# Optimization experiments

Hardware: AMD Instinct MI355X
Metric: run time of the kernel (lower is better)

## Reference

```python
import jax, jax.numpy as jnp
import numpy as np

B, N, D, H = 2, 2048, 1024, 16
HD = D // H

def setup_inputs() -> dict:
    key = jax.random.key(0)
    ks = jax.random.split(key, 8)
    s = lambda fan_in: 1.0 / np.sqrt(fan_in)
    return {
        "x": jax.random.normal(ks[0], (B, N, D), jnp.float32),
        "coverage": jax.random.uniform(ks[1], (B, N, 1), jnp.float32),
        "w_qkv": jax.random.normal(ks[2], (D, 3 * D), jnp.float32) * s(D),
        "w_out": jax.random.normal(ks[3], (D, D), jnp.float32) * s(D),
        "b_out": jnp.zeros((D,), jnp.float32),
        "w_ce1": jax.random.normal(ks[4], (1, D // 4), jnp.float32),
        "b_ce1": jnp.zeros((D // 4,), jnp.float32),
        "w_ce2": jax.random.normal(ks[5], (D // 4, H), jnp.float32) * s(D // 4),
        "b_ce2": jnp.zeros((H,), jnp.float32),
        "w_fg1": jax.random.normal(ks[6], (D, D // 4), jnp.float32) * s(D),
        "b_fg1": jnp.zeros((D // 4,), jnp.float32),
        "w_fg2": jax.random.normal(ks[7], (D // 4, 1), jnp.float32) * s(D // 4),
        "b_fg2": jnp.zeros((1,), jnp.float32),
    }

def reference(x, coverage, w_qkv, w_out, b_out, w_ce1, b_ce1, w_ce2, b_ce2,
              w_fg1, b_fg1, w_fg2, b_fg2):
    b, n, d = x.shape
    h = w_ce2.shape[1]
    hd = d // h
    scale = hd ** -0.5
    qkv = x @ w_qkv  # (B,N,3D)
    q, k, v = jnp.split(qkv, 3, axis=-1)
    q = q.reshape(b, n, h, hd).transpose(0, 2, 1, 3)  # (B,H,N,hd)
    k = k.reshape(b, n, h, hd).transpose(0, 2, 1, 3)
    v = v.reshape(b, n, h, hd).transpose(0, 2, 1, 3)
    attn = jnp.einsum("bhnd,bhmd->bhnm", q, k) * scale  # (B,H,N,N)
    # coverage bias: MLP(1 -> D/4 -> H), broadcast over query dim
    cov = jax.nn.silu(coverage @ w_ce1 + b_ce1) @ w_ce2 + b_ce2  # (B,N,H)
    cov_bias = cov.transpose(0, 2, 1)[:, :, None, :]  # (B,H,1,N)
    # fusion gate on mean-pooled features
    x_pooled = x.mean(axis=1)  # (B,D)
    g = jax.nn.sigmoid(jax.nn.silu(x_pooled @ w_fg1 + b_fg1) @ w_fg2 + b_fg2)  # (B,1)
    g = g[:, :, None, None]  # (B,1,1,1)
    # g*(attn+bias) + (1-g)*attn == attn + g*bias (exact same math)
    attn = attn + g * cov_bias
    attn = jax.nn.softmax(attn, axis=-1)
    out = jnp.einsum("bhnm,bhmd->bhnd", attn, v)  # (B,H,N,hd)
    out = out.transpose(0, 2, 1, 3).reshape(b, n, d)
    return out @ w_out + b_out
```

## Files before the change

kernel.cpp:

```cpp
#include <hip/hip_runtime.h>
#include <math.h>

typedef __bf16 bf16_t;
typedef __bf16 bf16x8 __attribute__((ext_vector_type(8)));
typedef __bf16 bf16x4 __attribute__((ext_vector_type(4)));
typedef float f32x4 __attribute__((ext_vector_type(4)));

#define MFMA16(a, b, c) __builtin_amdgcn_mfma_f32_16x16x32_bf16((a), (b), (c), 0, 0, 0)

constexpr int Bc = 2, Nc = 2048, Dc = 1024, Hc = 16, HDc = 64;
constexpr float C1 = 0.18033688011112042f;
constexpr float LOG2E = 1.4426950408889634f;

__device__ __forceinline__ void glds16(const bf16_t* g, bf16_t* l) {
    __builtin_amdgcn_global_load_lds(
        (const __attribute__((address_space(1))) unsigned int*)g,
        (__attribute__((address_space(3))) unsigned int*)l, 16, 0, 0);
}

__global__ __launch_bounds__(256) void f2b(const float* __restrict__ src,
                                           bf16_t* __restrict__ dst) {
    int i = (blockIdx.x * 256 + threadIdx.x) * 4;
    float4 v = *(const float4*)(src + i);
    bf16x4 o = { (bf16_t)v.x, (bf16_t)v.y, (bf16_t)v.z, (bf16_t)v.w };
    *(bf16x4*)(dst + i) = o;
}

__global__ __launch_bounds__(256) void tr64(const float* __restrict__ src,
                                            bf16_t* __restrict__ dst, int R, int C) {
    __shared__ bf16_t tile[64 * 66];
    int r0 = blockIdx.y * 64, c0 = blockIdx.x * 64;
    int t = threadIdx.x;
    int cl = t & 63, rl = t >> 6;
#pragma unroll
    for (int p = 0; p < 16; ++p) {
        int r = p * 4 + rl;
        tile[r * 66 + cl] = (bf16_t)src[(size_t)(r0 + r) * C + c0 + cl];
    }
    __syncthreads();
#pragma unroll
    for (int p = 0; p < 16; ++p) {
        int r = p * 4 + rl;
        dst[(size_t)(c0 + r) * R + r0 + cl] = tile[cl * 66 + r];
    }
}

__global__ __launch_bounds__(256) void pool_partial(const float* __restrict__ x,
                                                    float* __restrict__ pooled) {
    int blk = blockIdx.x;
    int b = blk >> 7, ch = blk & 127;
    int t = threadIdx.x;
    int c = t * 4;
    float s0 = 0.f, s1 = 0.f, s2 = 0.f, s3 = 0.f;
    for (int rr = 0; rr < 16; ++rr) {
        float4 v = *(const float4*)(x + (size_t)(b * Nc + ch * 16 + rr) * Dc + c);
        s0 += v.x; s1 += v.y; s2 += v.z; s3 += v.w;
    }
    atomicAdd(&pooled[b * Dc + c + 0], s0);
    atomicAdd(&pooled[b * Dc + c + 1], s1);
    atomicAdd(&pooled[b * Dc + c + 2], s2);
    atomicAdd(&pooled[b * Dc + c + 3], s3);
}

__global__ __launch_bounds__(256) void gate1(const float* __restrict__ pooled,
                                             const float* __restrict__ w_fg1,
                                             const float* __restrict__ b_fg1,
                                             const float* __restrict__ w_fg2,
                                             float* __restrict__ hacc) {
    int b = blockIdx.x >> 8, j = blockIdx.x & 255;
    int t = threadIdx.x;
    float p = 0.f;
#pragma unroll
    for (int i = 0; i < 4; ++i) {
        int d = t * 4 + i;
        p += pooled[b * 1024 + d] * w_fg1[d * 256 + j];
    }
#pragma unroll
    for (int off = 32; off > 0; off >>= 1) p += __shfl_down(p, off);
    __shared__ float red[4];
    if ((t & 63) == 0) red[t >> 6] = p;
    __syncthreads();
    if (t == 0) {
        float hj = (red[0] + red[1] + red[2] + red[3]) * (1.0f / 2048.0f) + b_fg1[j];
        hj = hj / (1.0f + __expf(-hj));
        atomicAdd(&hacc[b], hj * w_fg2[j]);
    }
}

__global__ __launch_bounds__(256) void covbias_k(const float* __restrict__ coverage,
                                                 const float* __restrict__ w_ce1,
                                                 const float* __restrict__ b_ce1,
                                                 const float* __restrict__ w_ce2,
                                                 const float* __restrict__ b_ce2,
                                                 const float* __restrict__ hacc,
                                                 const float* __restrict__ b_fg2,
                                                 float* __restrict__ biasbuf) {
    int t = threadIdx.x;
    int h = t & 15;
    int gn = blockIdx.x * 16 + (t >> 4);
    int b = gn >> 11, n = gn & 2047;
    float g = 1.0f / (1.0f + __expf(-(hacc[b] + b_fg2[0])));
    float c = coverage[gn];
    float acc = b_ce2[h];
    for (int j = 0; j < 256; ++j) {
        float tv = c * w_ce1[j] + b_ce1[j];
        tv = tv / (1.0f + __expf(-tv));
        acc += tv * w_ce2[j * 16 + h];
    }
    biasbuf[((size_t)b * 16 + h) * 2048 + n] = LOG2E * g * acc;
}

__global__ __launch_bounds__(256) void qkv_gemm(const bf16_t* __restrict__ Xb,
                                                const bf16_t* __restrict__ Wt,
                                                bf16_t* __restrict__ Q,
                                                bf16_t* __restrict__ Kb,
                                                bf16_t* __restrict__ Vt) {
    __shared__ __align__(16) bf16_t At[128 * 32];
    __shared__ __align__(16) bf16_t Bt[128 * 32];
    int t = threadIdx.x, w = t >> 6, lane = t & 63;
    int l16 = lane & 15, quad = lane >> 4;
    int wm = w & 1, wx = w >> 1;
    int m0 = blockIdx.x * 128;
    int n0 = blockIdx.y * 128;
    f32x4 acc[4][4] = {};
    int sw = (l16 >> 2) & 3;

    for (int k0 = 0; k0 < 1024; k0 += 32) {
#pragma unroll
        for (int i = 0; i < 2; ++i) {
            int fb = i * 4096 + w * 1024;
            int f = fb + lane * 16;
            int row = f >> 6;
            int ch = (f >> 4) & 3;
            int sc = ch ^ ((row >> 2) & 3);
            glds16(Wt + (size_t)(n0 + row) * 1024 + k0 + sc * 8, At + (fb >> 1));
            glds16(Xb + (size_t)(m0 + row) * 1024 + k0 + sc * 8, Bt + (fb >> 1));
        }
        __syncthreads();
        bf16x8 afr[4], bfr[4];
#pragma unroll
        for (int mi = 0; mi < 4; ++mi)
            afr[mi] = *(const bf16x8*)(At + (wm * 64 + mi * 16 + l16) * 32 + ((quad ^ sw) * 8));
#pragma unroll
        for (int ni = 0; ni < 4; ++ni)
            bfr[ni] = *(const bf16x8*)(Bt + (wx * 64 + ni * 16 + l16) * 32 + ((quad ^ sw) * 8));
#pragma unroll
        for (int mi = 0; mi < 4; ++mi)
#pragma unroll
            for (int ni = 0; ni < 4; ++ni)
                acc[mi][ni] = MFMA16(afr[mi], bfr[ni], acc[mi][ni]);
        __syncthreads();
    }

    int sec = n0 >> 10;
#pragma unroll
    for (int mi = 0; mi < 4; ++mi) {
        int gc = n0 + wm * 64 + mi * 16 + quad * 4;
        int dcol = gc & 1023;
        int h = dcol >> 6, hd = dcol & 63;
#pragma unroll
        for (int ni = 0; ni < 4; ++ni) {
            int gx = m0 + wx * 64 + ni * 16 + l16;
            int b = gx >> 11, n = gx & 2047;
            size_t bh = (size_t)(b * 16 + h);
            if (sec == 2) {
#pragma unroll
                for (int r = 0; r < 4; ++r)
                    Vt[(bh * 64 + hd + r) * 2048 + n] = (bf16_t)acc[mi][ni][r];
            } else {
                bf16x4 pk = { (bf16_t)acc[mi][ni][0], (bf16_t)acc[mi][ni][1],
                              (bf16_t)acc[mi][ni][2], (bf16_t)acc[mi][ni][3] };
                bf16_t* dst = (sec == 0 ? Q : Kb);
                *(bf16x4*)(dst + (bh * 2048 + n) * 64 + hd) = pk;
            }
        }
    }
}

__global__ __launch_bounds__(256) void attn_k(const bf16_t* __restrict__ Q,
                                              const bf16_t* __restrict__ Kb,
                                              const bf16_t* __restrict__ Vt,
                                              const float* __restrict__ biasbuf,
                                              bf16_t* __restrict__ O) {
    __shared__ __align__(16) bf16_t kbuf[2][64 * 64];
    __shared__ __align__(16) bf16_t vbuf[2][64 * 64];
    int t = threadIdx.x, w = t >> 6, lane = t & 63;
    int l16 = lane & 15, quad = lane >> 4;
    int bh = blockIdx.y;
    int b = bh >> 4, h = bh & 15;
    int qa = blockIdx.x * 64 + w * 16;
    const bf16_t* Qh = Q + (size_t)bh * 2048 * 64;
    const bf16_t* Kh = Kb + (size_t)bh * 2048 * 64;
    const bf16_t* Vh = Vt + (size_t)bh * 64 * 2048;
    const float* bih = biasbuf + (size_t)bh * 2048;

    int fb0 = w * 2048, fb1 = fb0 + 1024;
    int f0 = fb0 + lane * 16, f1 = fb1 + lane * 16;
    int krow0 = f0 >> 7, kch0 = ((f0 >> 4) & 7) ^ (krow0 & 7);
    int krow1 = f1 >> 7, kch1 = ((f1 >> 4) & 7) ^ (krow1 & 7);

    bf16x8 qf[2];
#pragma unroll
    for (int dh = 0; dh < 2; ++dh)
        qf[dh] = *(const bf16x8*)(Qh + (size_t)(qa + l16) * 64 + dh * 32 + quad * 8);

    f32x4 o[4] = {};
    float lsum = 0.f;
    const f32x4 zero = { 0.f, 0.f, 0.f, 0.f };
    int swl = l16 & 7;
    int qh = quad >> 1, ql = quad & 1;

    {
        glds16(Kh + (size_t)krow0 * 64 + kch0 * 8, &kbuf[0][fb0 >> 1]);
        glds16(Kh + (size_t)krow1 * 64 + kch1 * 8, &kbuf[0][fb1 >> 1]);
        glds16(Vh + (size_t)krow0 * 2048 + kch0 * 8, &vbuf[0][fb0 >> 1]);
        glds16(Vh + (size_t)krow1 * 2048 + kch1 * 8, &vbuf[0][fb1 >> 1]);
    }

    for (int it = 0; it < 32; ++it) {
        int j0 = it * 64, sel = it & 1;
        __syncthreads();
        if (it + 1 < 32) {
            int jn = j0 + 64, sn = sel ^ 1;
            glds16(Kh + (size_t)(jn + krow0) * 64 + kch0 * 8, &kbuf[sn][fb0 >> 1]);
            glds16(Kh + (size_t)(jn + krow1) * 64 + kch1 * 8, &kbuf[sn][fb1 >> 1]);
            glds16(Vh + (size_t)krow0 * 2048 + jn + kch0 * 8, &vbuf[sn][fb0 >> 1]);
            glds16(Vh + (size_t)krow1 * 2048 + jn + kch1 * 8, &vbuf[sn][fb1 >> 1]);
        }
        const bf16_t* kb = kbuf[sel];
        const bf16_t* vb = vbuf[sel];

        float4 bias[4];
#pragma unroll
        for (int kt = 0; kt < 4; ++kt)
            bias[kt] = *(const float4*)(bih + j0 + kt * 16 + quad * 4);

        f32x4 s[4];
#pragma unroll
        for (int kt = 0; kt < 4; ++kt) {
            bf16x8 kf0 = *(const bf16x8*)(kb + (kt * 16 + l16) * 64 + ((quad ^ swl) * 8));
            bf16x8 kf1 = *(const bf16x8*)(kb + (kt * 16 + l16) * 64 + (((4 + quad) ^ swl) * 8));
            s[kt] = MFMA16(kf0, qf[0], zero);
            s[kt] = MFMA16(kf1, qf[1], s[kt]);
        }

#pragma unroll
        for (int kt = 0; kt < 4; ++kt) {
            const float* bp = (const float*)&bias[kt];
#pragma unroll
            for (int r = 0; r < 4; ++r) {
                float p = __builtin_amdgcn_exp2f(s[kt][r] * C1 + bp[r]);
                s[kt][r] = p;
                lsum += p;
            }
        }

        bf16x8 pf[2];
#pragma unroll
        for (int pv = 0; pv < 2; ++pv) {
            bf16x8 tmp;
#pragma unroll
            for (int i = 0; i < 4; ++i) {
                tmp[i]     = (bf16_t)s[2 * pv][i];
                tmp[i + 4] = (bf16_t)s[2 * pv + 1][i];
            }
            pf[pv] = tmp;
        }

#pragma unroll
        for (int dt = 0; dt < 4; ++dt) {
            const bf16_t* vrow = vb + (dt * 16 + l16) * 64 + ql * 4;
#pragma unroll
            for (int pv = 0; pv < 2; ++pv) {
                int c0 = (pv * 4 + qh) ^ swl;
                int c1 = (pv * 4 + 2 + qh) ^ swl;
                bf16x4 va = *(const bf16x4*)(vrow + c0 * 8);
                bf16x4 vc = *(const bf16x4*)(vrow + c1 * 8);
                bf16x8 vf = __builtin_shufflevector(va, vc, 0, 1, 2, 3, 4, 5, 6, 7);
                o[dt] = MFMA16(pf[pv], vf, o[dt]);
            }
        }
    }

    lsum += __shfl_xor(lsum, 16);
    lsum += __shfl_xor(lsum, 32);
    float rinv[4];
#pragma unroll
    for (int r = 0; r < 4; ++r)
        rinv[r] = 1.0f / __shfl(lsum, quad * 4 + r);
#pragma unroll
    for (int dt = 0; dt < 4; ++dt)
#pragma unroll
        for (int r = 0; r < 4; ++r) {
            int row = qa + quad * 4 + r;
            O[(size_t)(b * 2048 + row) * 1024 + h * 64 + dt * 16 + l16] =
                (bf16_t)(o[dt][r] * rinv[r]);
        }
}

__global__ __launch_bounds__(256) void out_gemm(const bf16_t* __restrict__ A,
                                                const bf16_t* __restrict__ Wt,
                                                const float* __restrict__ bias,
                                                float* __restrict__ Cout) {
    __shared__ __align__(16) bf16_t At[128 * 32];
    __shared__ __align__(16) bf16_t Bt[128 * 32];
    int t = threadIdx.x, w = t >> 6, lane = t & 63;
    int l16 = lane & 15, quad = lane >> 4;
    int wm = w & 1, wx = w >> 1;
    int m0 = blockIdx.x * 128;
    int n0 = blockIdx.y * 128;
    f32x4 acc[4][4] = {};
    int sw = (l16 >> 2) & 3;

    for (int k0 = 0; k0 < 1024; k0 += 32) {
#pragma unroll
        for (int i = 0; i < 2; ++i) {
            int fb = i * 4096 + w * 1024;
            int f = fb + lane * 16;
            int row = f >> 6;
            int ch = (f >> 4) & 3;
            int sc = ch ^ ((row >> 2) & 3);
            glds16(Wt + (size_t)(n0 + row) * 1024 + k0 + sc * 8, At + (fb >> 1));
            glds16(A + (size_t)(m0 + row) * 1024 + k0 + sc * 8, Bt + (fb >> 1));
        }
        __syncthreads();
        bf16x8 afr[4], bfr[4];
#pragma unroll
        for (int mi = 0; mi < 4; ++mi)
            afr[mi] = *(const bf16x8*)(At + (wm * 64 + mi * 16 + l16) * 32 + ((quad ^ sw) * 8));
#pragma unroll
        for (int ni = 0; ni < 4; ++ni)
            bfr[ni] = *(const bf16x8*)(Bt + (wx * 64 + ni * 16 + l16) * 32 + ((quad ^ sw) * 8));
#pragma unroll
        for (int mi = 0; mi < 4; ++mi)
#pragma unroll
            for (int ni = 0; ni < 4; ++ni)
                acc[mi][ni] = MFMA16(afr[mi], bfr[ni], acc[mi][ni]);
        __syncthreads();
    }

#pragma unroll
    for (int mi = 0; mi < 4; ++mi) {
        int gc = n0 + wm * 64 + mi * 16 + quad * 4;
        float4 bv = *(const float4*)(bias + gc);
#pragma unroll
        for (int ni = 0; ni < 4; ++ni) {
            int gx = m0 + wx * 64 + ni * 16 + l16;
            float4 ov = { acc[mi][ni][0] + bv.x, acc[mi][ni][1] + bv.y,
                          acc[mi][ni][2] + bv.z, acc[mi][ni][3] + bv.w };
            *(float4*)(Cout + (size_t)gx * 1024 + gc) = ov;
        }
    }
}

extern "C" void kernel_launch(void* const* d_in, const int* in_sizes, int n_in,
                              void* d_out, int out_size, void* d_ws, size_t ws_size,
                              hipStream_t stream) {
    const float* x     = (const float*)d_in[0];
    const float* cov   = (const float*)d_in[1];
    const float* w_qkv = (const float*)d_in[2];
    const float* w_out = (const float*)d_in[3];
    const float* b_out = (const float*)d_in[4];
    const float* w_ce1 = (const float*)d_in[5];
    const float* b_ce1 = (const float*)d_in[6];
    const float* w_ce2 = (const float*)d_in[7];
    const float* b_ce2 = (const float*)d_in[8];
    const float* w_fg1 = (const float*)d_in[9];
    const float* b_fg1 = (const float*)d_in[10];
    const float* w_fg2 = (const float*)d_in[11];
    const float* b_fg2 = (const float*)d_in[12];

    char* ws = (char*)d_ws;
    bf16_t* Wt     = (bf16_t*)(ws);
    bf16_t* WoT    = (bf16_t*)(ws + 6291456);
    bf16_t* Xb     = (bf16_t*)(ws + 8388608);
    bf16_t* Qb     = (bf16_t*)(ws + 16777216);
    bf16_t* Kbb    = (bf16_t*)(ws + 25165824);
    bf16_t* Vt     = (bf16_t*)(ws + 33554432);
    bf16_t* Ob     = (bf16_t*)(ws + 41943040);
    float*  pooled = (float*)(ws + 50331648);
    float*  hacc   = (float*)(ws + 50339840);
    float*  biasb  = (float*)(ws + 50340096);

    hipMemsetAsync(pooled, 0, 2 * 1024 * sizeof(float), stream);
    hipMemsetAsync(hacc, 0, 2 * sizeof(float), stream);
    f2b<<<4096, 256, 0, stream>>>(x, Xb);
    tr64<<<dim3(48, 16), 256, 0, stream>>>(w_qkv, Wt, 1024, 3072);
    tr64<<<dim3(16, 16), 256, 0, stream>>>(w_out, WoT, 1024, 1024);
    pool_partial<<<256, 256, 0, stream>>>(x, pooled);
    gate1<<<512, 256, 0, stream>>>(pooled, w_fg1, b_fg1, w_fg2, hacc);
    covbias_k<<<256, 256, 0, stream>>>(cov, w_ce1, b_ce1, w_ce2, b_ce2, hacc, b_fg2, biasb);
    qkv_gemm<<<dim3(32, 24), 256, 0, stream>>>(Xb, Wt, Qb, Kbb, Vt);
    attn_k<<<dim3(32, 32), 256, 0, stream>>>(Qb, Kbb, Vt, biasb, Ob);
    out_gemm<<<dim3(32, 8), 256, 0, stream>>>(Ob, WoT, b_out, (float*)d_out);
}
```

Before: 278.8 us.

## Process two query tiles per wave and fold scale and bias into MFMA

```diff
diff --git a/kernel.cpp b/kernel.cpp
--- a/kernel.cpp
+++ b/kernel.cpp
@@ -153,6 +153,7 @@
     }
 
     int sec = n0 >> 10;
+    float scq = (sec == 0) ? C1 : 1.0f;
 #pragma unroll
     for (int mi = 0; mi < 4; ++mi) {
         int gc = n0 + wm * 64 + mi * 16 + quad * 4;
@@ -168,8 +169,8 @@
                 for (int r = 0; r < 4; ++r)
                     Vt[(bh * 64 + hd + r) * 2048 + n] = (bf16_t)acc[mi][ni][r];
             } else {
-                bf16x4 pk = { (bf16_t)acc[mi][ni][0], (bf16_t)acc[mi][ni][1],
-                              (bf16_t)acc[mi][ni][2], (bf16_t)acc[mi][ni][3] };
+                bf16x4 pk = { (bf16_t)(acc[mi][ni][0] * scq), (bf16_t)(acc[mi][ni][1] * scq),
+                              (bf16_t)(acc[mi][ni][2] * scq), (bf16_t)(acc[mi][ni][3] * scq) };
                 bf16_t* dst = (sec == 0 ? Q : Kb);
                 *(bf16x4*)(dst + (bh * 2048 + n) * 64 + hd) = pk;
             }
@@ -188,7 +189,7 @@
     int l16 = lane & 15, quad = lane >> 4;
     int bh = blockIdx.y;
     int b = bh >> 4, h = bh & 15;
-    int qa = blockIdx.x * 64 + w * 16;
+    int qa = blockIdx.x * 128 + w * 32;
     const bf16_t* Qh = Q + (size_t)bh * 2048 * 64;
     const bf16_t* Kh = Kb + (size_t)bh * 2048 * 64;
     const bf16_t* Vh = Vt + (size_t)bh * 64 * 2048;
@@ -199,14 +200,18 @@
     int krow0 = f0 >> 7, kch0 = ((f0 >> 4) & 7) ^ (krow0 & 7);
     int krow1 = f1 >> 7, kch1 = ((f1 >> 4) & 7) ^ (krow1 & 7);
 
-    bf16x8 qf[2];
-#pragma unroll
-    for (int dh = 0; dh < 2; ++dh)
-        qf[dh] = *(const bf16x8*)(Qh + (size_t)(qa + l16) * 64 + dh * 32 + quad * 8);
-
-    f32x4 o[4] = {};
-    float lsum = 0.f;
-    const f32x4 zero = { 0.f, 0.f, 0.f, 0.f };
+    bf16x8 qf[2][2];
+#pragma unroll
+    for (int qt = 0; qt < 2; ++qt)
+#pragma unroll
+        for (int dh = 0; dh < 2; ++dh)
+            qf[qt][dh] = *(const bf16x8*)(Qh + (size_t)(qa + qt * 16 + l16) * 64 + dh * 32 + quad * 8);
+
+    f32x4 o[2][4] = {};
+    f32x4 lacc[2] = {};
+    bf16x8 onesb;
+#pragma unroll
+    for (int i = 0; i < 8; ++i) onesb[i] = (bf16_t)1.0f;
     int swl = l16 & 7;
     int qh = quad >> 1, ql = quad & 1;
 
@@ -230,41 +235,44 @@
         const bf16_t* kb = kbuf[sel];
         const bf16_t* vb = vbuf[sel];
 
-        float4 bias[4];
+        float4 b4[4];
 #pragma unroll
         for (int kt = 0; kt < 4; ++kt)
-            bias[kt] = *(const float4*)(bih + j0 + kt * 16 + quad * 4);
-
-        f32x4 s[4];
+            b4[kt] = *(const float4*)(bih + j0 + kt * 16 + quad * 4);
+
+        f32x4 s[2][4];
 #pragma unroll
         for (int kt = 0; kt < 4; ++kt) {
+            f32x4 bi = { b4[kt].x, b4[kt].y, b4[kt].z, b4[kt].w };
             bf16x8 kf0 = *(const bf16x8*)(kb + (kt * 16 + l16) * 64 + ((quad ^ swl) * 8));
             bf16x8 kf1 = *(const bf16x8*)(kb + (kt * 16 + l16) * 64 + (((4 + quad) ^ swl) * 8));
-            s[kt] = MFMA16(kf0, qf[0], zero);
-            s[kt] = MFMA16(kf1, qf[1], s[kt]);
-        }
-
-#pragma unroll
-        for (int kt = 0; kt < 4; ++kt) {
-            const float* bp = (const float*)&bias[kt];
-#pragma unroll
-            for (int r = 0; r < 4; ++r) {
-                float p = __builtin_amdgcn_exp2f(s[kt][r] * C1 + bp[r]);
-                s[kt][r] = p;
-                lsum += p;
+#pragma unroll
+            for (int qt = 0; qt < 2; ++qt) {
+                s[qt][kt] = MFMA16(kf0, qf[qt][0], bi);
+                s[qt][kt] = MFMA16(kf1, qf[qt][1], s[qt][kt]);
             }
         }
 
-        bf16x8 pf[2];
-#pragma unroll
-        for (int pv = 0; pv < 2; ++pv) {
-            bf16x8 tmp;
-#pragma unroll
-            for (int i = 0; i < 4; ++i) {
-                tmp[i]     = (bf16_t)s[2 * pv][i];
-                tmp[i + 4] = (bf16_t)s[2 * pv + 1][i];
+        bf16x8 pf[2][2];
+#pragma unroll
+        for (int qt = 0; qt < 2; ++qt) {
+#pragma unroll
+            for (int kt = 0; kt < 4; ++kt)
+#pragma unroll
+                for (int r = 0; r < 4; ++r)
+                    s[qt][kt][r] = __builtin_amdgcn_exp2f(s[qt][kt][r]);
+#pragma unroll
+            for (int pv = 0; pv < 2; ++pv) {
+                bf16x8 tmp;
+#pragma unroll
+                for (int i = 0; i < 4; ++i) {
+                    tmp[i]     = (bf16_t)s[qt][2 * pv][i];
+                    tmp[i + 4] = (bf16_t)s[qt][2 * pv + 1][i];
+                }
+                pf[qt][pv] = tmp;
             }
-            pf[pv] = tmp;
+            lacc[qt] = MFMA16(pf[qt][0], onesb, lacc[qt]);
+            lacc[qt] = MFMA16(pf[qt][1], onesb, lacc[qt]);
         }
 
 #pragma unroll
@@ -277,25 +285,27 @@
                 bf16x4 va = *(const bf16x4*)(vrow + c0 * 8);
                 bf16x4 vc = *(const bf16x4*)(vrow + c1 * 8);
                 bf16x8 vf = __builtin_shufflevector(va, vc, 0, 1, 2, 3, 4, 5, 6, 7);
-                o[dt] = MFMA16(pf[pv], vf, o[dt]);
+#pragma unroll
+                for (int qt = 0; qt < 2; ++qt)
+                    o[qt][dt] = MFMA16(pf[qt][pv], vf, o[qt][dt]);
             }
         }
     }
 
-    lsum += __shfl_xor(lsum, 16);
-    lsum += __shfl_xor(lsum, 32);
-    float rinv[4];
-#pragma unroll
-    for (int r = 0; r < 4; ++r)
-        rinv[r] = 1.0f / __shfl(lsum, quad * 4 + r);
-#pragma unroll
-    for (int dt = 0; dt < 4; ++dt)
-#pragma unroll
-        for (int r = 0; r < 4; ++r) {
-            int row = qa + quad * 4 + r;
-            O[(size_t)(b * 2048 + row) * 1024 + h * 64 + dt * 16 + l16] =
-                (bf16_t)(o[dt][r] * rinv[r]);
-        }
+#pragma unroll
+    for (int qt = 0; qt < 2; ++qt) {
+        f32x4 rinv;
+#pragma unroll
+        for (int r = 0; r < 4; ++r) rinv[r] = 1.0f / lacc[qt][r];
+#pragma unroll
+        for (int dt = 0; dt < 4; ++dt)
+#pragma unroll
+            for (int r = 0; r < 4; ++r) {
+                int row = qa + qt * 16 + quad * 4 + r;
+                O[(size_t)(b * 2048 + row) * 1024 + h * 64 + dt * 16 + l16] =
+                    (bf16_t)(o[qt][dt][r] * rinv[r]);
+            }
+    }
 }
 
 __global__ __launch_bounds__(256) void out_gemm(const bf16_t* __restrict__ A,
@@ -391,6 +401,6 @@
     gate1<<<512, 256, 0, stream>>>(pooled, w_fg1, b_fg1, w_fg2, hacc);
     covbias_k<<<256, 256, 0, stream>>>(cov, w_ce1, b_ce1, w_ce2, b_ce2, hacc, b_fg2, biasb);
     qkv_gemm<<<dim3(32, 24), 256, 0, stream>>>(Xb, Wt, Qb, Kbb, Vt);
-    attn_k<<<dim3(32, 32), 256, 0, stream>>>(Qb, Kbb, Vt, biasb, Ob);
+    attn_k<<<dim3(16, 32), 256, 0, stream>>>(Qb, Kbb, Vt, biasb, Ob);
     out_gemm<<<dim3(32, 8), 256, 0, stream>>>(Ob, WoT, b_out, (float*)d_out);
 }
```

Result: faster. 269.1 us (-3.5%).
